# Kernel tuning notes

Measured on AMD Instinct MI355X. Metric: run time of the kernel, lower is better.

## Reference

```python
import jax, jax.numpy as jnp
import numpy as np

N_SRC0, N_DST0, N_DST1 = 400000, 200000, 100000
E0, E1 = 3200000, 1600000
IN_FEATS, H_FEATS, NUM_CLASSES, NUM_CELL_TYPES = 128, 256, 8, 24


def setup_inputs() -> dict:
    key = jax.random.key(0)
    ks = jax.random.split(key, 12)
    feats = jax.random.normal(ks[0], (N_SRC0, IN_FEATS), dtype=jnp.float32)
    cell_ids = jax.random.randint(ks[1], (N_SRC0,), 0, NUM_CELL_TYPES)
    x = jnp.concatenate([cell_ids.astype(jnp.float32)[:, None], feats], axis=1)  # [N,129]
    src0 = jax.random.randint(ks[2], (E0,), 0, N_SRC0, dtype=jnp.int32)
    dst0 = jax.random.randint(ks[3], (E0,), 0, N_DST0, dtype=jnp.int32)
    src1 = jax.random.randint(ks[4], (E1,), 0, N_DST0, dtype=jnp.int32)
    dst1 = jax.random.randint(ks[5], (E1,), 0, N_DST1, dtype=jnp.int32)
    s = 1.0 / np.sqrt(IN_FEATS)
    s2 = 1.0 / np.sqrt(H_FEATS)
    return {
        "x": x,
        "src0": src0, "dst0": dst0, "src1": src1, "dst1": dst1,
        "n_dst0": N_DST0, "n_dst1": N_DST1,
        "emb": jax.random.normal(ks[6], (NUM_CELL_TYPES, IN_FEATS), dtype=jnp.float32),
        "W_self1": jax.random.normal(ks[7], (IN_FEATS, H_FEATS), dtype=jnp.float32) * s,
        "W_neigh1": jax.random.normal(ks[8], (IN_FEATS, H_FEATS), dtype=jnp.float32) * s,
        "b1": jnp.zeros((H_FEATS,), dtype=jnp.float32),
        "W_self2": jax.random.normal(ks[9], (H_FEATS, NUM_CLASSES), dtype=jnp.float32) * s2,
        "W_neigh2": jax.random.normal(ks[10], (H_FEATS, NUM_CLASSES), dtype=jnp.float32) * s2,
        "b2": jnp.zeros((NUM_CLASSES,), dtype=jnp.float32),
    }


def _sage_mean(h_src, h_dst, src, dst, n_dst, W_self, W_neigh, b):
    # gather src features along edges, mean-reduce onto dst nodes
    msg = h_src[src]                                                # [E, d]
    agg = jax.ops.segment_sum(msg, dst, num_segments=n_dst)        # [n_dst, d]
    deg = jax.ops.segment_sum(jnp.ones_like(dst, dtype=h_src.dtype), dst, num_segments=n_dst)
    agg = agg / jnp.maximum(deg, 1.0)[:, None]
    return h_dst @ W_self + agg @ W_neigh + b


def reference(x, src0, dst0, src1, dst1, n_dst0, n_dst1,
              emb, W_self1, W_neigh1, b1, W_self2, W_neigh2, b2):
    cell_ids = x[:, 0].astype(jnp.int32)
    feat = x[:, 1:]
    h = feat * jax.nn.sigmoid(emb[cell_ids])  # embedding-gated features; dropout = identity (eval)
    h_dst = h[:n_dst0]
    h1 = jax.nn.relu(_sage_mean(h, h_dst, src0, dst0, n_dst0, W_self1, W_neigh1, b1))
    h1_dst = h1[:n_dst1]
    out = _sage_mean(h1, h1_dst, src1, dst1, n_dst1, W_self2, W_neigh2, b2)
    return out
```

## Files before the change

### kernel.cpp

```cpp
#include <hip/hip_runtime.h>

typedef unsigned int uint;
typedef unsigned short ushort;
typedef __attribute__((ext_vector_type(8))) short short8;
typedef __attribute__((ext_vector_type(4))) float f32x4;

__device__ __forceinline__ float bflo(uint u) { return __uint_as_float(u << 16); }
__device__ __forceinline__ float bfhi(uint u) { return __uint_as_float(u & 0xffff0000u); }
__device__ __forceinline__ ushort f2bf(float f) {
    uint u = __float_as_uint(f);
    u += 0x7fffu + ((u >> 16) & 1u);
    return (ushort)(u >> 16);
}
__device__ __forceinline__ uint pack2(float a, float b) {
    return (uint)f2bf(a) | ((uint)f2bf(b) << 16);
}
__device__ __forceinline__ float sigm(float e) { return 1.0f / (1.0f + __expf(-e)); }

#define ND0 200000
#define ND1 100000
#define INF 128
#define HF  256
#define BCAP 24576

__global__ __launch_bounds__(256) void gate_k(const float* __restrict__ x,
                                              const float* __restrict__ emb,
                                              ushort* __restrict__ h, int nnodes) {
    int tid  = blockIdx.x * 256 + threadIdx.x;
    int node = tid >> 4, tq = tid & 15;
    if (node >= nnodes) return;
    const float* xr = x + (size_t)node * 129;
    int cell = (int)xr[0];
    int f0 = tq * 8;
    const float* er = emb + cell * INF + f0;
    float4 e0 = *(const float4*)er;
    float4 e1 = *(const float4*)(er + 4);
    float v[8];
    __builtin_memcpy(&v[0], xr + 1 + f0, 16);
    __builtin_memcpy(&v[4], xr + 5 + f0, 16);
    uint4 o;
    o.x = pack2(v[0] * sigm(e0.x), v[1] * sigm(e0.y));
    o.y = pack2(v[2] * sigm(e0.z), v[3] * sigm(e0.w));
    o.z = pack2(v[4] * sigm(e1.x), v[5] * sigm(e1.y));
    o.w = pack2(v[6] * sigm(e1.z), v[7] * sigm(e1.w));
    *(uint4*)(h + (size_t)node * INF + f0) = o;
}

#define SCAN_B 1024
__global__ __launch_bounds__(256) void scan1_k(const int* __restrict__ in,
                                               int* __restrict__ out,
                                               int* __restrict__ bsum, int n) {
    __shared__ int tmp[256];
    int t = threadIdx.x;
    int base = blockIdx.x * SCAN_B;
    int v[4], s = 0;
#pragma unroll
    for (int q = 0; q < 4; ++q) {
        int idx = base + t * 4 + q;
        v[q] = (idx < n) ? ((in[idx] + 3) & ~3) : 0;
        s += v[q];
    }
    tmp[t] = s; __syncthreads();
    for (int off = 1; off < 256; off <<= 1) {
        int xv = (t >= off) ? tmp[t - off] : 0; __syncthreads();
        tmp[t] += xv; __syncthreads();
    }
    int excl = tmp[t] - s;
#pragma unroll
    for (int q = 0; q < 4; ++q) {
        int idx = base + t * 4 + q;
        if (idx < n) out[idx] = excl;
        excl += v[q];
    }
    if (t == 255) bsum[blockIdx.x] = tmp[255];
}

__global__ __launch_bounds__(256) void scan2_k(int* __restrict__ bsum, int nb) {
    __shared__ int tmp[256];
    int t = threadIdx.x;
    int s = (t < nb) ? bsum[t] : 0;
    tmp[t] = s; __syncthreads();
    for (int off = 1; off < 256; off <<= 1) {
        int xv = (t >= off) ? tmp[t - off] : 0; __syncthreads();
        tmp[t] += xv; __syncthreads();
    }
    if (t < nb) bsum[t] = tmp[t] - s;
}

__global__ __launch_bounds__(256) void scan3_k(int* __restrict__ row_start,
                                               const int* __restrict__ bsum, int n) {
    int i = blockIdx.x * blockDim.x + threadIdx.x;
    if (i < n) row_start[i] += bsum[i >> 10];
}

__global__ __launch_bounds__(256) void binA_k(const int* __restrict__ src,
                                              const int* __restrict__ dst,
                                              uint* __restrict__ pairs,
                                              int* __restrict__ gcur,
                                              int* __restrict__ cnt, int E) {
    __shared__ int hist[256];
    __shared__ int curs[256];
    const int CHUNK = 4096;
    int t = threadIdx.x;
    for (int c0 = blockIdx.x * CHUNK; c0 < E; c0 += gridDim.x * CHUNK) {
        int n = min(CHUNK, E - c0);
        hist[t] = 0;
        __syncthreads();
        for (int i = t; i < n; i += 256) atomicAdd(&hist[dst[c0 + i] >> 10], 1);
        __syncthreads();
        curs[t] = hist[t] ? atomicAdd(&gcur[t], hist[t]) : 0;
        __syncthreads();
        for (int i = t; i < n; i += 256) {
            int d = dst[c0 + i];
            atomicAdd(&cnt[d], 1);
            int b = d >> 10;
            int p = atomicAdd(&curs[b], 1);
            pairs[(size_t)b * BCAP + p] = ((uint)src[c0 + i] << 10) | (uint)(d & 1023);
        }
        __syncthreads();
    }
}

__global__ __launch_bounds__(256) void binB_k(const uint* __restrict__ pairs,
                                              const int* __restrict__ gcur,
                                              const int* __restrict__ row_start,
                                              int* __restrict__ csr, int nd, int zrow) {
    __shared__ int cur[1024];
    int b = blockIdx.x, t = threadIdx.x;
    int dbase = b << 10;
    for (int i = t; i < 1024; i += 256)
        cur[i] = (dbase + i < nd) ? row_start[dbase + i] : 0;
    __syncthreads();
    int ne = gcur[b];
    const uint* bp = pairs + (size_t)b * BCAP;
    for (int i = t; i < ne; i += 256) {
        uint e = bp[i];
        int p = atomicAdd(&cur[e & 1023], 1);
        csr[p] = (int)(e >> 10);
    }
    __syncthreads();
    for (int i = t; i < 1024; i += 256) {
        if (dbase + i >= nd) continue;
        int pe = cur[i];
        int pad = (-(pe - row_start[dbase + i])) & 3;
        for (int q = 0; q < pad; ++q) csr[pe + q] = zrow;
    }
}

__global__ __launch_bounds__(256) void gather4_k(const int* __restrict__ csr,
                                                 const int* __restrict__ row_start,
                                                 const int* __restrict__ cnt,
                                                 const ushort* __restrict__ hsrc,
                                                 uint* __restrict__ aggm, int nrows) {
    int w    = (blockIdx.x * blockDim.x + threadIdx.x) >> 6;
    int lane = threadIdx.x & 63;
    if (w >= nrows) return;
    int beg = row_start[w], c = cnt[w];
    int end = beg + ((c + 3) & ~3);
    const uint* hb = (const uint*)hsrc;
    float a0 = 0.f, a1 = 0.f;
    for (int j = beg; j < end; j += 4) {
        int4 s4 = *(const int4*)(csr + j);
        uint u0 = hb[(size_t)s4.x * 64 + lane];
        uint u1 = hb[(size_t)s4.y * 64 + lane];
        uint u2 = hb[(size_t)s4.z * 64 + lane];
        uint u3 = hb[(size_t)s4.w * 64 + lane];
        a0 += (bflo(u0) + bflo(u1)) + (bflo(u2) + bflo(u3));
        a1 += (bfhi(u0) + bfhi(u1)) + (bfhi(u2) + bfhi(u3));
    }
    float inv = 1.0f / fmaxf((float)c, 1.0f);
    aggm[(size_t)w * 64 + lane] = pack2(a0 * inv, a1 * inv);
}

__global__ __launch_bounds__(256) void wconv_k(const float* __restrict__ Ws,
                                               const float* __restrict__ Wn,
                                               uint* __restrict__ Wb) {
    int tid  = blockIdx.x * 256 + threadIdx.x;
    int lane = tid & 63, nf = (tid >> 6) & 15, ks = tid >> 10;
    int n  = nf * 16 + (lane & 15);
    int k0 = ks * 32 + ((lane >> 4) << 3);
    uint o[4];
#pragma unroll
    for (int p = 0; p < 4; ++p) {
        int k = k0 + 2 * p;
        float a = (k < 128)     ? Ws[(size_t)k * HF + n]       : Wn[(size_t)(k - 128) * HF + n];
        float b = (k + 1 < 128) ? Ws[(size_t)(k + 1) * HF + n] : Wn[(size_t)(k - 127) * HF + n];
        o[p] = pack2(a, b);
    }
    uint4 v = { o[0], o[1], o[2], o[3] };
    *(uint4*)(Wb + (size_t)tid * 4) = v;
}

__global__ __launch_bounds__(256) void wpack2_k(const float* __restrict__ Ws2,
                                                const float* __restrict__ Wn2,
                                                uint* __restrict__ Wb2) {
    int tid = blockIdx.x * 256 + threadIdx.x;
    if (tid >= 512) return;
    int lane = tid & 63, ks = tid >> 6;
    int n  = lane & 15;
    int k0 = ks * 32 + ((lane >> 4) << 3);
    const float* W = (n < 8) ? Wn2 : Ws2;
    int c = n & 7;
    uint o[4];
#pragma unroll
    for (int p = 0; p < 4; ++p) {
        int k = k0 + 2 * p;
        o[p] = pack2(W[(size_t)k * 8 + c], W[(size_t)(k + 1) * 8 + c]);
    }
    uint4 v = { o[0], o[1], o[2], o[3] };
    *(uint4*)(Wb2 + (size_t)tid * 4) = v;
}

__global__ __launch_bounds__(256) void layer1_mfma_k(const uint* __restrict__ hb,
                                                     const uint* __restrict__ aggm,
                                                     const uint* __restrict__ Wb,
                                                     const uint* __restrict__ Wb2,
                                                     const float* __restrict__ b1,
                                                     float* __restrict__ z,
                                                     float* __restrict__ out, int nd1) {
    __shared__ uint lds[64 * 132];
    int t = threadIdx.x, lane = t & 63, wid = t >> 6;
    int quad = lane >> 4, l16 = lane & 15;
    int r0 = blockIdx.x * 64;

#pragma unroll
    for (int it = 0; it < 8; ++it) {
        int i = t + it * 256;
        int r = i >> 5, u4 = i & 31;
        const uint* src = (u4 < 16) ? (hb + (size_t)(r0 + r) * 64 + u4 * 4)
                                    : (aggm + (size_t)(r0 + r) * 64 + (u4 - 16) * 4);
        *(uint4*)&lds[r * 132 + u4 * 4] = *(const uint4*)src;
    }

    float bias[4];
#pragma unroll
    for (int i = 0; i < 4; ++i) bias[i] = b1[wid * 64 + i * 16 + l16];
    f32x4 acc[4][4];
#pragma unroll
    for (int mf = 0; mf < 4; ++mf)
#pragma unroll
        for (int i = 0; i < 4; ++i)
            acc[mf][i] = (f32x4){ bias[i], bias[i], bias[i], bias[i] };

    __syncthreads();

#pragma unroll
    for (int ks = 0; ks < 8; ++ks) {
        short8 bfr[4];
#pragma unroll
        for (int i = 0; i < 4; ++i) {
            int nf = wid * 4 + i;
            bfr[i] = *(const short8*)(Wb + (size_t)((ks * 16 + nf) * 64 + lane) * 4);
        }
        short8 afr[4];
#pragma unroll
        for (int mf = 0; mf < 4; ++mf) {
            int r = mf * 16 + l16;
            afr[mf] = *(const short8*)&lds[r * 132 + ks * 16 + quad * 4];
        }
#pragma unroll
        for (int mf = 0; mf < 4; ++mf)
#pragma unroll
            for (int i = 0; i < 4; ++i)
                acc[mf][i] = __builtin_amdgcn_mfma_f32_16x16x32_bf16(afr[mf], bfr[i],
                                                                     acc[mf][i], 0, 0, 0);
    }

    __syncthreads();
    ushort* st = (ushort*)lds;
#pragma unroll
    for (int mf = 0; mf < 4; ++mf)
#pragma unroll
        for (int i = 0; i < 4; ++i) {
            int col = wid * 64 + i * 16 + l16;
#pragma unroll
            for (int reg = 0; reg < 4; ++reg) {
                int row = mf * 16 + quad * 4 + reg;
                st[row * 264 + col] = f2bf(fmaxf(acc[mf][i][reg], 0.0f));
            }
        }
    __syncthreads();

    f32x4 zacc = (f32x4){ 0.f, 0.f, 0.f, 0.f };
    int rloc = wid * 16 + l16;
#pragma unroll
    for (int ks = 0; ks < 8; ++ks) {
        short8 a = *(const short8*)&lds[rloc * 132 + ks * 16 + quad * 4];
        short8 b = *(const short8*)(Wb2 + (size_t)(ks * 64 + lane) * 4);
        zacc = __builtin_amdgcn_mfma_f32_16x16x32_bf16(a, b, zacc, 0, 0, 0);
    }
#pragma unroll
    for (int reg = 0; reg < 4; ++reg) {
        int r = r0 + wid * 16 + quad * 4 + reg;
        if (l16 < 8) z[(size_t)r * 8 + l16] = zacc[reg];
        else if (r < nd1) out[(size_t)r * 8 + (l16 - 8)] = zacc[reg];
    }
}

__global__ __launch_bounds__(256) void gz_k(const int* __restrict__ csr,
                                            const int* __restrict__ row_start,
                                            const int* __restrict__ cnt,
                                            const float* __restrict__ z,
                                            const float* __restrict__ b2,
                                            float* __restrict__ out, int nrows) {
    int tid = blockIdx.x * 256 + threadIdx.x;
    int d = tid >> 3, c = tid & 7;
    if (d >= nrows) return;
    int beg = row_start[d], n = cnt[d];
    int end = beg + ((n + 3) & ~3);
    float a = 0.f;
    for (int j = beg; j < end; j += 4) {
        int4 s4 = *(const int4*)(csr + j);
        a += z[(size_t)s4.x * 8 + c] + z[(size_t)s4.y * 8 + c]
           + z[(size_t)s4.z * 8 + c] + z[(size_t)s4.w * 8 + c];
    }
    float inv = 1.0f / fmaxf((float)n, 1.0f);
    out[(size_t)d * 8 + c] += a * inv + b2[c];
}

extern "C" void kernel_launch(void* const* d_in, const int* in_sizes, int n_in,
                              void* d_out, int out_size, void* d_ws, size_t ws_size,
                              hipStream_t stream) {
    const float* x    = (const float*)d_in[0];
    const int*   src0 = (const int*)d_in[1];
    const int*   dst0 = (const int*)d_in[2];
    const int*   src1 = (const int*)d_in[3];
    const int*   dst1 = (const int*)d_in[4];
    const float* emb  = (const float*)d_in[7];
    const float* Ws1  = (const float*)d_in[8];
    const float* Wn1  = (const float*)d_in[9];
    const float* b1   = (const float*)d_in[10];
    const float* Ws2  = (const float*)d_in[11];
    const float* Wn2  = (const float*)d_in[12];
    const float* b2   = (const float*)d_in[13];
    int E0 = in_sizes[1];
    int E1 = in_sizes[3];
    int nsrc = in_sizes[0] / 129;

    char* p = (char*)d_ws;
    ushort* h         = (ushort*)p;  p += ((size_t)nsrc + 1) * INF * 2;
    uint*   aggm      = (uint*)p;    p += (size_t)ND0 * 64 * 4;
    int*    csr       = (int*)p;     p += ((size_t)E0 + 3 * (size_t)ND0 + 16) * 4;
    int*    cnt       = (int*)p;     p += (size_t)ND0 * 4;
    int*    row_start = (int*)p;     p += (size_t)ND0 * 4;
    int*    bsum      = (int*)p;     p += 256 * 4;
    int*    gcur      = (int*)p;     p += 256 * 4;
    uint*   Wb        = (uint*)p;    p += 8192 * 16;
    uint*   Wb2       = (uint*)p;    p += 512 * 16;
    float*  z         = (float*)p;   p += ((size_t)ND0 + 1) * 8 * 4;
    uint*   pairs     = aggm;

    int ZR0 = nsrc;
    int ZR1 = ND0;

    hipMemsetAsync(cnt, 0, (size_t)ND0 * 4, stream);
    hipMemsetAsync(gcur, 0, 256 * 4, stream);
    hipMemsetAsync(h + (size_t)ZR0 * INF, 0, INF * 2, stream);
    gate_k<<<(nsrc * 16 + 255) / 256, 256, 0, stream>>>(x, emb, h, nsrc);
    wconv_k<<<32, 256, 0, stream>>>(Ws1, Wn1, Wb);
    wpack2_k<<<2, 256, 0, stream>>>(Ws2, Wn2, Wb2);
    int nb0 = (ND0 + SCAN_B - 1) / SCAN_B;
    binA_k<<<512, 256, 0, stream>>>(src0, dst0, pairs, gcur, cnt, E0);
    scan1_k<<<nb0, 256, 0, stream>>>(cnt, row_start, bsum, ND0);
    scan2_k<<<1, 256, 0, stream>>>(bsum, nb0);
    scan3_k<<<(ND0 + 255) / 256, 256, 0, stream>>>(row_start, bsum, ND0);
    binB_k<<<nb0, 256, 0, stream>>>(pairs, gcur, row_start, csr, ND0, ZR0);
    gather4_k<<<(ND0 + 3) / 4, 256, 0, stream>>>(csr, row_start, cnt, h, aggm, ND0);
    layer1_mfma_k<<<ND0 / 64, 256, 0, stream>>>((const uint*)h, aggm, Wb, Wb2, b1,
                                                z, (float*)d_out, ND1);

    hipMemsetAsync(cnt, 0, (size_t)ND1 * 4, stream);
    hipMemsetAsync(gcur, 0, 256 * 4, stream);
    hipMemsetAsync(z + (size_t)ZR1 * 8, 0, 8 * 4, stream);
    int nb1 = (ND1 + SCAN_B - 1) / SCAN_B;
    binA_k<<<512, 256, 0, stream>>>(src1, dst1, pairs, gcur, cnt, E1);
    scan1_k<<<nb1, 256, 0, stream>>>(cnt, row_start, bsum, ND1);
    scan2_k<<<1, 256, 0, stream>>>(bsum, nb1);
    scan3_k<<<(ND1 + 255) / 256, 256, 0, stream>>>(row_start, bsum, ND1);
    binB_k<<<nb1, 256, 0, stream>>>(pairs, gcur, row_start, csr, ND1, ZR1);
    gz_k<<<(ND1 * 8 + 255) / 256, 256, 0, stream>>>(csr, row_start, cnt, z, b2,
                                                    (float*)d_out, ND1);
}
```

Baseline: 877.3 us.

## Single-pass edge binning with vectorized loads, padded counters, wider binB blocks

The bucketing kernel now reads dst and src with 128-bit loads, eight edges per thread. It records each edge's local rank from a single shared-histogram atomic, so the old second pass of shared cursor atomics and the second dst read go away. Global bucket counters are padded to a stride of 16 ints to avoid contention on shared cache lines. The grid grows to one block per 2048-edge chunk, and the CSR fill kernel uses 1024-thread blocks, one thread per destination row. This adds register pressure for the per-edge metadata, and the packed rank field assumes chunks of at most 2048 edges.

```diff
diff --git a/kernel.cpp b/kernel.cpp
--- a/kernel.cpp
+++ b/kernel.cpp
@@ -22,6 +22,7 @@
 #define INF 128
 #define HF  256
 #define BCAP 24576
+#define GSTRIDE 16
 
 __global__ __launch_bounds__(256) void gate_k(const float* __restrict__ x,
                                               const float* __restrict__ emb,
@@ -93,56 +94,95 @@
     if (i < n) row_start[i] += bsum[i >> 10];
 }
 
+#define CHUNK_A 2048
 __global__ __launch_bounds__(256) void binA_k(const int* __restrict__ src,
                                               const int* __restrict__ dst,
                                               uint* __restrict__ pairs,
                                               int* __restrict__ gcur,
                                               int* __restrict__ cnt, int E) {
     __shared__ int hist[256];
-    __shared__ int curs[256];
-    const int CHUNK = 4096;
+    __shared__ int base[256];
     int t = threadIdx.x;
-    for (int c0 = blockIdx.x * CHUNK; c0 < E; c0 += gridDim.x * CHUNK) {
-        int n = min(CHUNK, E - c0);
+    for (int c0 = blockIdx.x * CHUNK_A; c0 < E; c0 += gridDim.x * CHUNK_A) {
+        int n = min(CHUNK_A, E - c0);
         hist[t] = 0;
         __syncthreads();
-        for (int i = t; i < n; i += 256) atomicAdd(&hist[dst[c0 + i] >> 10], 1);
-        __syncthreads();
-        curs[t] = hist[t] ? atomicAdd(&gcur[t], hist[t]) : 0;
-        __syncthreads();
-        for (int i = t; i < n; i += 256) {
-            int d = dst[c0 + i];
-            atomicAdd(&cnt[d], 1);
-            int b = d >> 10;
-            int p = atomicAdd(&curs[b], 1);
-            pairs[(size_t)b * BCAP + p] = ((uint)src[c0 + i] << 10) | (uint)(d & 1023);
+        int i0 = t * 8;
+        uint meta[8];
+        if (i0 + 8 <= n) {
+            int4 da = *(const int4*)(dst + c0 + i0);
+            int4 db = *(const int4*)(dst + c0 + i0 + 4);
+            int dv[8] = { da.x, da.y, da.z, da.w, db.x, db.y, db.z, db.w };
+#pragma unroll
+            for (int q = 0; q < 8; ++q) {
+                int d = dv[q];
+                atomicAdd(&cnt[d], 1);
+                int b = d >> 10;
+                int r = atomicAdd(&hist[b], 1);
+                meta[q] = ((uint)b << 21) | ((uint)r << 10) | (uint)(d & 1023);
+            }
+        } else {
+#pragma unroll
+            for (int q = 0; q < 8; ++q) {
+                int i = i0 + q;
+                if (i < n) {
+                    int d = dst[c0 + i];
+                    atomicAdd(&cnt[d], 1);
+                    int b = d >> 10;
+                    int r = atomicAdd(&hist[b], 1);
+                    meta[q] = ((uint)b << 21) | ((uint)r << 10) | (uint)(d & 1023);
+                } else meta[q] = 0xFFFFFFFFu;
+            }
         }
         __syncthreads();
-    }
-}
-
-__global__ __launch_bounds__(256) void binB_k(const uint* __restrict__ pairs,
-                                              const int* __restrict__ gcur,
-                                              const int* __restrict__ row_start,
-                                              int* __restrict__ csr, int nd, int zrow) {
+        base[t] = hist[t] ? atomicAdd(&gcur[t * GSTRIDE], hist[t]) : 0;
+        __syncthreads();
+        if (i0 + 8 <= n) {
+            int4 sa = *(const int4*)(src + c0 + i0);
+            int4 sb = *(const int4*)(src + c0 + i0 + 4);
+            int sv[8] = { sa.x, sa.y, sa.z, sa.w, sb.x, sb.y, sb.z, sb.w };
+#pragma unroll
+            for (int q = 0; q < 8; ++q) {
+                uint m = meta[q];
+                uint b = m >> 21;
+                uint p = (uint)base[b] + ((m >> 10) & 2047u);
+                pairs[(size_t)b * BCAP + p] = ((uint)sv[q] << 10) | (m & 1023u);
+            }
+        } else {
+#pragma unroll
+            for (int q = 0; q < 8; ++q) {
+                uint m = meta[q];
+                if (m != 0xFFFFFFFFu) {
+                    uint b = m >> 21;
+                    uint p = (uint)base[b] + ((m >> 10) & 2047u);
+                    pairs[(size_t)b * BCAP + p] = ((uint)src[c0 + i0 + q] << 10) | (m & 1023u);
+                }
+            }
+        }
+        __syncthreads();
+    }
+}
+
+__global__ __launch_bounds__(1024) void binB_k(const uint* __restrict__ pairs,
+                                               const int* __restrict__ gcur,
+                                               const int* __restrict__ row_start,
+                                               int* __restrict__ csr, int nd, int zrow) {
     __shared__ int cur[1024];
     int b = blockIdx.x, t = threadIdx.x;
     int dbase = b << 10;
-    for (int i = t; i < 1024; i += 256)
-        cur[i] = (dbase + i < nd) ? row_start[dbase + i] : 0;
+    cur[t] = (dbase + t < nd) ? row_start[dbase + t] : 0;
     __syncthreads();
-    int ne = gcur[b];
+    int ne = gcur[b * GSTRIDE];
     const uint* bp = pairs + (size_t)b * BCAP;
-    for (int i = t; i < ne; i += 256) {
+    for (int i = t; i < ne; i += 1024) {
         uint e = bp[i];
         int p = atomicAdd(&cur[e & 1023], 1);
         csr[p] = (int)(e >> 10);
     }
     __syncthreads();
-    for (int i = t; i < 1024; i += 256) {
-        if (dbase + i >= nd) continue;
-        int pe = cur[i];
-        int pad = (-(pe - row_start[dbase + i])) & 3;
+    if (dbase + t < nd) {
+        int pe = cur[t];
+        int pad = (-(pe - row_start[dbase + t])) & 3;
         for (int q = 0; q < pad; ++q) csr[pe + q] = zrow;
     }
 }
@@ -344,7 +384,7 @@
     int*    cnt       = (int*)p;     p += (size_t)ND0 * 4;
     int*    row_start = (int*)p;     p += (size_t)ND0 * 4;
     int*    bsum      = (int*)p;     p += 256 * 4;
-    int*    gcur      = (int*)p;     p += 256 * 4;
+    int*    gcur      = (int*)p;     p += 256 * GSTRIDE * 4;
     uint*   Wb        = (uint*)p;    p += 8192 * 16;
     uint*   Wb2       = (uint*)p;    p += 512 * 16;
     float*  z         = (float*)p;   p += ((size_t)ND0 + 1) * 8 * 4;
@@ -354,30 +394,32 @@
     int ZR1 = ND0;
 
     hipMemsetAsync(cnt, 0, (size_t)ND0 * 4, stream);
-    hipMemsetAsync(gcur, 0, 256 * 4, stream);
+    hipMemsetAsync(gcur, 0, 256 * GSTRIDE * 4, stream);
     hipMemsetAsync(h + (size_t)ZR0 * INF, 0, INF * 2, stream);
     gate_k<<<(nsrc * 16 + 255) / 256, 256, 0, stream>>>(x, emb, h, nsrc);
     wconv_k<<<32, 256, 0, stream>>>(Ws1, Wn1, Wb);
     wpack2_k<<<2, 256, 0, stream>>>(Ws2, Wn2, Wb2);
     int nb0 = (ND0 + SCAN_B - 1) / SCAN_B;
-    binA_k<<<512, 256, 0, stream>>>(src0, dst0, pairs, gcur, cnt, E0);
+    int ch0 = (E0 + CHUNK_A - 1) / CHUNK_A;
+    binA_k<<<min(ch0, 2048), 256, 0, stream>>>(src0, dst0, pairs, gcur, cnt, E0);
     scan1_k<<<nb0, 256, 0, stream>>>(cnt, row_start, bsum, ND0);
     scan2_k<<<1, 256, 0, stream>>>(bsum, nb0);
     scan3_k<<<(ND0 + 255) / 256, 256, 0, stream>>>(row_start, bsum, ND0);
-    binB_k<<<nb0, 256, 0, stream>>>(pairs, gcur, row_start, csr, ND0, ZR0);
+    binB_k<<<nb0, 1024, 0, stream>>>(pairs, gcur, row_start, csr, ND0, ZR0);
     gather4_k<<<(ND0 + 3) / 4, 256, 0, stream>>>(csr, row_start, cnt, h, aggm, ND0);
     layer1_mfma_k<<<ND0 / 64, 256, 0, stream>>>((const uint*)h, aggm, Wb, Wb2, b1,
                                                 z, (float*)d_out, ND1);
 
     hipMemsetAsync(cnt, 0, (size_t)ND1 * 4, stream);
-    hipMemsetAsync(gcur, 0, 256 * 4, stream);
+    hipMemsetAsync(gcur, 0, 256 * GSTRIDE * 4, stream);
     hipMemsetAsync(z + (size_t)ZR1 * 8, 0, 8 * 4, stream);
     int nb1 = (ND1 + SCAN_B - 1) / SCAN_B;
-    binA_k<<<512, 256, 0, stream>>>(src1, dst1, pairs, gcur, cnt, E1);
+    int ch1 = (E1 + CHUNK_A - 1) / CHUNK_A;
+    binA_k<<<min(ch1, 2048), 256, 0, stream>>>(src1, dst1, pairs, gcur, cnt, E1);
     scan1_k<<<nb1, 256, 0, stream>>>(cnt, row_start, bsum, ND1);
     scan2_k<<<1, 256, 0, stream>>>(bsum, nb1);
     scan3_k<<<(ND1 + 255) / 256, 256, 0, stream>>>(row_start, bsum, ND1);
-    binB_k<<<nb1, 256, 0, stream>>>(pairs, gcur, row_start, csr, ND1, ZR1);
+    binB_k<<<nb1, 1024, 0, stream>>>(pairs, gcur, row_start, csr, ND1, ZR1);
     gz_k<<<(ND1 * 8 + 255) / 256, 256, 0, stream>>>(csr, row_start, cnt, z, b2,
                                                     (float*)d_out, ND1);
 }
```

Measured after the change: 855.1 us. -2.5%, faster.
